# Kernel tuning notes

Measured on AMD Instinct MI355X. Metric: run time of the kernel, lower is better.

The kernel has to match this reference:

```python
import jax, jax.numpy as jnp
import numpy as np
from jax import lax

V, E, H, MLP, NCLS = 50000, 100, 100, 300, 3
B, T, C = 256, 128, 255


def _lstm_dir(x, Wih, Whh, bih, bhh, reverse):
    # x: [T, B, E]; PyTorch gate order i, f, g, o
    Bsz = x.shape[1]
    h0 = jnp.zeros((Bsz, H), x.dtype)
    c0 = jnp.zeros((Bsz, H), x.dtype)

    def step(carry, xt):
        h, c = carry
        gates = xt @ Wih.T + h @ Whh.T + (bih + bhh)  # [B, 4H]
        i, f, g, o = jnp.split(gates, 4, axis=-1)
        c = jax.nn.sigmoid(f) * c + jax.nn.sigmoid(i) * jnp.tanh(g)
        h = jax.nn.sigmoid(o) * jnp.tanh(c)
        return (h, c), h

    _, hs = lax.scan(step, (h0, c0), x, reverse=reverse)
    return hs  # [T, B, H]


def setup_inputs() -> dict:
    key = jax.random.key(0)
    ks = jax.random.split(key, 16)
    s_e = 1.0 / np.sqrt(H)
    inp = {
        "x": jax.random.randint(ks[0], (B, T), 0, V),
        "paths": jax.random.randint(ks[1], (B, C, 3), 0, T),
        "emb": jax.random.normal(ks[2], (V, E), jnp.float32),
        "Wih_f": jax.random.uniform(ks[3], (4 * H, E), jnp.float32, -s_e, s_e),
        "Whh_f": jax.random.uniform(ks[4], (4 * H, H), jnp.float32, -s_e, s_e),
        "bih_f": jax.random.uniform(ks[5], (4 * H,), jnp.float32, -s_e, s_e),
        "bhh_f": jax.random.uniform(ks[6], (4 * H,), jnp.float32, -s_e, s_e),
        "Wih_b": jax.random.uniform(ks[7], (4 * H, E), jnp.float32, -s_e, s_e),
        "Whh_b": jax.random.uniform(ks[8], (4 * H, H), jnp.float32, -s_e, s_e),
        "bih_b": jax.random.uniform(ks[9], (4 * H,), jnp.float32, -s_e, s_e),
        "bhh_b": jax.random.uniform(ks[10], (4 * H,), jnp.float32, -s_e, s_e),
        "W1": jax.random.normal(ks[11], (6 * H, MLP), jnp.float32) * 0.05,
        "b1": jnp.zeros((MLP,), jnp.float32),
        "W2": jax.random.normal(ks[12], (MLP, NCLS), jnp.float32) * 0.05,
        "b2": jnp.zeros((NCLS,), jnp.float32),
    }
    return inp


def reference(x, paths, emb, Wih_f, Whh_f, bih_f, bhh_f, Wih_b, Whh_b, bih_b, bhh_b, W1, b1, W2, b2):
    # embedding lookup (dropout is eval-mode identity)
    xe = emb[x]                      # [B, T, E]
    xe = jnp.transpose(xe, (1, 0, 2))  # [T, B, E] (seq-major like packed LSTM)
    hf = _lstm_dir(xe, Wih_f, Whh_f, bih_f, bhh_f, reverse=False)
    hb = _lstm_dir(xe, Wih_b, Whh_b, bih_b, bhh_b, reverse=True)
    h = jnp.concatenate([hf, hb], axis=-1)        # [T, B, 2H]
    hbt = jnp.transpose(h, (1, 0, 2))             # [B, T, 2H]
    # gather 3 positions per configuration; index -1 -> zero vector
    idx = jnp.clip(paths, 0, T - 1)               # [B, C, 3]
    g = hbt[jnp.arange(hbt.shape[0])[:, None, None], idx]  # [B, C, 3, 2H]
    g = jnp.where((paths >= 0)[..., None], g, 0.0)
    mlp_in = g.reshape(-1, 6 * H)                 # [B*C, 600]
    hdn = jnp.tanh(mlp_in @ W1 + b1)
    return jax.nn.softmax(hdn @ W2 + b2, axis=-1)  # [B*C, 3]
```

## Files before the change

### kernel.cpp

```cpp
#include <hip/hip_runtime.h>

typedef unsigned short u16;
typedef short short8 __attribute__((ext_vector_type(8)));
typedef float f32x4 __attribute__((ext_vector_type(4)));

__device__ __forceinline__ u16 f2b(float x){
  union{float f; unsigned u;} v; v.f = x;
  unsigned r = (v.u + 0x7FFFu + ((v.u >> 16) & 1u)) >> 16;
  return (u16)r;
}
__device__ __forceinline__ u16 f2h(float x){
  union{_Float16 h; u16 u;} c; c.h = (_Float16)x; return c.u;
}
__device__ __forceinline__ float b2f(u16 h){
  union{unsigned u; float f;} v; v.u = ((unsigned)h) << 16; return v.f;
}
__device__ __forceinline__ float sigm(float x){ return 1.0f/(1.0f + __expf(-x)); }
__device__ __forceinline__ float tanh_f(float x){ return 1.0f - 2.0f/(1.0f + __expf(2.0f*x)); }

__global__ void prep_kernel(const int* __restrict__ x, const float* __restrict__ emb,
   const float* __restrict__ Wih_f, const float* __restrict__ Whh_f,
   const float* __restrict__ bih_f, const float* __restrict__ bhh_f,
   const float* __restrict__ Wih_b, const float* __restrict__ Whh_b,
   const float* __restrict__ bih_b, const float* __restrict__ bhh_b,
   const float* __restrict__ W1,
   u16* __restrict__ xe, u16* __restrict__ wc, float* __restrict__ biasC,
   u16* __restrict__ whh2, u16* __restrict__ w1b, u16* __restrict__ hbt)
{
  int id = blockIdx.x*256 + threadIdx.x;
  const int N0 = 32768*128;
  const int N1 = 832*128;
  const int N2 = 800;
  const int N3 = 102400;
  const int N4 = 672*320;
  const int N5 = 32768*24;
  if (id < N0){
    int p = id >> 7, k = id & 127;
    float v = 0.f;
    if (k < 100) v = emb[x[p]*100 + k];
    xe[id] = f2b(v);
    return;
  }
  id -= N0;
  if (id < N1){
    int n = id >> 7, k = id & 127;
    float v = 0.f;
    if (k < 100){
      if (n < 400) v = Wih_f[n*100+k];
      else if (n < 800) v = Wih_b[(n-400)*100+k];
    }
    wc[id] = f2b(v);
    return;
  }
  id -= N1;
  if (id < N2){
    biasC[id] = (id < 400) ? (bih_f[id]+bhh_f[id]) : (bih_b[id-400]+bhh_b[id-400]);
    return;
  }
  id -= N2;
  if (id < N3){
    int d = id / 51200; int rem = id - d*51200;
    int t = rem >> 7;  int e  = rem & 127;
    int g = e >> 5;    int kq = e & 31;
    int u = t >> 2;    int q  = t & 3;
    int k = q*32 + kq;
    float v = 0.f;
    if (k < 100){
      const float* W = d ? Whh_b : Whh_f;
      v = W[(g*100 + u)*100 + k];
    }
    whh2[id] = f2h(v);
    return;
  }
  id -= N3;
  if (id < N4){
    int k = id / 320; int n = id - k*320;
    int seg = k / 224; int wwk = k - seg*224;
    float v = 0.f;
    if (n < 300 && wwk < 200) v = W1[(seg*200 + wwk)*300 + n];
    w1b[n*672 + k] = f2b(v);
    return;
  }
  id -= N4;
  if (id < N5){
    int p = id / 24; int k = id - p*24;
    hbt[p*224 + 200 + k] = 0;
  }
}

__global__ __launch_bounds__(256) void gemm1_kernel(const u16* __restrict__ xe,
    const u16* __restrict__ wc, const float* __restrict__ biasC, u16* __restrict__ inp)
{
  __shared__ __align__(16) u16 As[64*136];
  __shared__ __align__(16) u16 Bs[64*136];
  const int m0 = blockIdx.x*64, n0 = blockIdx.y*64;
  const int tid = threadIdx.x;
  #pragma unroll
  for (int i=0;i<4;i++){
    int f = i*256 + tid;
    int row = f >> 4, c8 = f & 15;
    *(uint4*)&As[row*136 + c8*8] = *(const uint4*)&xe[(m0+row)*128 + c8*8];
    *(uint4*)&Bs[row*136 + c8*8] = *(const uint4*)&wc[(n0+row)*128 + c8*8];
  }
  __syncthreads();
  const int w = tid >> 6, lane = tid & 63, col = lane & 15, quad = lane >> 4;
  f32x4 acc[4];
  #pragma unroll
  for (int nt=0;nt<4;nt++) acc[nt] = (f32x4){0.f,0.f,0.f,0.f};
  #pragma unroll
  for (int kc=0;kc<4;kc++){
    short8 af = *(const short8*)&As[(w*16+col)*136 + kc*32 + quad*8];
    #pragma unroll
    for (int nt=0;nt<4;nt++){
      short8 bfrag = *(const short8*)&Bs[(nt*16+col)*136 + kc*32 + quad*8];
      acc[nt] = __builtin_amdgcn_mfma_f32_16x16x32_bf16(af, bfrag, acc[nt], 0, 0, 0);
    }
  }
  #pragma unroll
  for (int nt=0;nt<4;nt++){
    int n = n0 + nt*16 + col;
    if (n < 800){
      float bs = biasC[n];
      int dir = (n >= 400) ? 1 : 0;
      int j = n - dir*400;
      int gg = j / 100, uu = j - gg*100;
      int pj = uu*4 + gg;
      #pragma unroll
      for (int r=0;r<4;r++){
        int m = m0 + w*16 + quad*4 + r;
        inp[(dir*32768 + m)*400 + pj] = f2b(acc[nt][r] + bs);
      }
    }
  }
}

#define DSL(CNT, H0,H1,H2,H3, A0,A1,A2,A3, B0,B1,B2,B3, C0,C1,C2,C3, D0,D1,D2,D3) \
  "s_waitcnt lgkmcnt(" #CNT ")\n\t" \
  "v_dot2_f32_f16 v16, v" #A0 ", v" #H0 ", v16\n\t" \
  "v_dot2_f32_f16 v17, v" #B0 ", v" #H0 ", v17\n\t" \
  "v_dot2_f32_f16 v18, v" #C0 ", v" #H0 ", v18\n\t" \
  "v_dot2_f32_f16 v19, v" #D0 ", v" #H0 ", v19\n\t" \
  "v_dot2_f32_f16 v16, v" #A1 ", v" #H1 ", v16\n\t" \
  "v_dot2_f32_f16 v17, v" #B1 ", v" #H1 ", v17\n\t" \
  "v_dot2_f32_f16 v18, v" #C1 ", v" #H1 ", v18\n\t" \
  "v_dot2_f32_f16 v19, v" #D1 ", v" #H1 ", v19\n\t" \
  "v_dot2_f32_f16 v16, v" #A2 ", v" #H2 ", v16\n\t" \
  "v_dot2_f32_f16 v17, v" #B2 ", v" #H2 ", v17\n\t" \
  "v_dot2_f32_f16 v18, v" #C2 ", v" #H2 ", v18\n\t" \
  "v_dot2_f32_f16 v19, v" #D2 ", v" #H2 ", v19\n\t" \
  "v_dot2_f32_f16 v16, v" #A3 ", v" #H3 ", v16\n\t" \
  "v_dot2_f32_f16 v17, v" #B3 ", v" #H3 ", v17\n\t" \
  "v_dot2_f32_f16 v18, v" #C3 ", v" #H3 ", v18\n\t" \
  "v_dot2_f32_f16 v19, v" #D3 ", v" #H3 ", v19\n\t"

__global__ __launch_bounds__(448) void lstm_kernel(const u16* __restrict__ inp,
    const u16* __restrict__ whh2, u16* __restrict__ hbt)
{
  __shared__ __align__(512) u16 hs2[256];
  const int cid = blockIdx.x;
  const int b = cid & 255, dir = cid >> 8;
  const int tid = threadIdx.x;
  for (int i = tid; i < 128; i += 448) ((float*)hs2)[i] = 0.f;
  __syncthreads();
  if (tid < 400){
    unsigned long long fe  = __ballot(1);
    unsigned long long g0e = __ballot((tid & 3) == 0);
    unsigned long long g1e = __ballot((tid & 3) == 1);
    const int sw  = tid >> 6;
    const int t0  = dir ? 127 : 0;
    const int dIb = dir ? -800 : 800;
    const int dHb = dir ? -448 : 448;
    const int swb = dir*102400;
    const unsigned sio = (unsigned)((dir*32768 + b*128 + t0)*400) * 2u;
    const unsigned sho = (unsigned)((b*128 + t0)*224 + dir*100) * 2u;
    const unsigned sra = (unsigned)(size_t)&hs2[0];
    const unsigned sha = sra + 256u;
    asm volatile(
      "v_mbcnt_lo_u32_b32 v0, -1, 0\n\t"
      "v_mbcnt_hi_u32_b32 v0, -1, v0\n\t"
      "v_lshl_add_u32 v0, %[sw], 6, v0\n\t"
      "v_lshlrev_b32 v1, 8, v0\n\t"
      "v_add_u32 v1, %[swb], v1\n\t"
      "v_lshrrev_b32 v3, 2, v0\n\t"
      "v_and_b32 v2, 3, v0\n\t"
      "v_lshl_add_u32 v23, v2, 6, %[sra]\n\t"
      "v_lshl_add_u32 v24, v3, 1, %[sha]\n\t"
      "v_lshl_add_u32 v25, v3, 1, %[sho]\n\t"
      "v_lshl_add_u32 v26, v3, 3, %[sio]\n\t"
      "v_mov_b32 v22, 0\n\t"
      "s_mov_b32 s20, 128\n\t"
      "global_load_dwordx2 v[20:21], v26, %[ib]\n\t"
      "v_add_u32 v26, %[dis], v26\n\t"
      "global_load_dwordx4 v[32:35], v1, %[wb]\n\t"
      "global_load_dwordx4 v[36:39], v1, %[wb] offset:16\n\t"
      "global_load_dwordx4 v[40:43], v1, %[wb] offset:32\n\t"
      "global_load_dwordx4 v[44:47], v1, %[wb] offset:48\n\t"
      "global_load_dwordx4 v[48:51], v1, %[wb] offset:64\n\t"
      "global_load_dwordx4 v[52:55], v1, %[wb] offset:80\n\t"
      "global_load_dwordx4 v[56:59], v1, %[wb] offset:96\n\t"
      "global_load_dwordx4 v[60:63], v1, %[wb] offset:112\n\t"
      "global_load_dwordx4 v[64:67], v1, %[wb] offset:128\n\t"
      "global_load_dwordx4 v[68:71], v1, %[wb] offset:144\n\t"
      "global_load_dwordx4 v[72:75], v1, %[wb] offset:160\n\t"
      "global_load_dwordx4 v[76:79], v1, %[wb] offset:176\n\t"
      "global_load_dwordx4 v[80:83], v1, %[wb] offset:192\n\t"
      "global_load_dwordx4 v[84:87], v1, %[wb] offset:208\n\t"
      "global_load_dwordx4 v[88:91], v1, %[wb] offset:224\n\t"
      "global_load_dwordx4 v[92:95], v1, %[wb] offset:240\n\t"
      "LSTM_T%=:\n\t"
      "s_waitcnt vmcnt(0)\n\t"
      "v_lshlrev_b32 v27, 16, v20\n\t"
      "v_and_b32 v28, 0xffff0000, v20\n\t"
      "v_lshlrev_b32 v29, 16, v21\n\t"
      "v_and_b32 v30, 0xffff0000, v21\n\t"
      "global_load_dwordx2 v[20:21], v26, %[ib]\n\t"
      "v_add_u32 v26, %[dis], v26\n\t"
      "ds_read_b128 v[0:3], v23\n\t"
      "ds_read_b128 v[4:7], v23 offset:16\n\t"
      "ds_read_b128 v[8:11], v23 offset:32\n\t"
      "ds_read_b128 v[12:15], v23 offset:48\n\t"
      "v_mov_b32 v16, 0\n\t"
      "v_mov_b32 v17, 0\n\t"
      "v_mov_b32 v18, 0\n\t"
      "v_mov_b32 v19, 0\n\t"
      DSL(3, 0,1,2,3,     32,33,34,35, 48,49,50,51, 64,65,66,67, 80,81,82,83)
      DSL(2, 4,5,6,7,     36,37,38,39, 52,53,54,55, 68,69,70,71, 84,85,86,87)
      DSL(1, 8,9,10,11,   40,41,42,43, 56,57,58,59, 72,73,74,75, 88,89,90,91)
      DSL(0, 12,13,14,15, 44,45,46,47, 60,61,62,63, 76,77,78,79, 92,93,94,95)
      "s_nop 1\n\t"
      "v_add_f32_dpp v16, v16, v16 quad_perm:[1,0,3,2] row_mask:0xf bank_mask:0xf\n\t"
      "v_add_f32_dpp v17, v17, v17 quad_perm:[1,0,3,2] row_mask:0xf bank_mask:0xf\n\t"
      "v_add_f32_dpp v18, v18, v18 quad_perm:[1,0,3,2] row_mask:0xf bank_mask:0xf\n\t"
      "v_add_f32_dpp v19, v19, v19 quad_perm:[1,0,3,2] row_mask:0xf bank_mask:0xf\n\t"
      "v_add_f32_dpp v16, v16, v16 quad_perm:[2,3,0,1] row_mask:0xf bank_mask:0xf\n\t"
      "v_add_f32_dpp v17, v17, v17 quad_perm:[2,3,0,1] row_mask:0xf bank_mask:0xf\n\t"
      "v_add_f32_dpp v18, v18, v18 quad_perm:[2,3,0,1] row_mask:0xf bank_mask:0xf\n\t"
      "v_add_f32_dpp v19, v19, v19 quad_perm:[2,3,0,1] row_mask:0xf bank_mask:0xf\n\t"
      "v_add_f32 v16, v16, v27\n\t"
      "v_add_f32 v17, v17, v28\n\t"
      "v_add_f32 v18, v18, v29\n\t"
      "v_add_f32 v19, v19, v30\n\t"
      "v_mul_f32 v27, 0xbfb8aa3b, v17\n\t"
      "v_mul_f32 v28, 0xbfb8aa3b, v16\n\t"
      "v_mul_f32 v29, 0x4038aa3b, v18\n\t"
      "v_exp_f32 v27, v27\n\t"
      "v_exp_f32 v28, v28\n\t"
      "v_exp_f32 v29, v29\n\t"
      "v_add_f32 v27, 1.0, v27\n\t"
      "v_add_f32 v28, 1.0, v28\n\t"
      "v_add_f32 v29, 1.0, v29\n\t"
      "v_rcp_f32 v27, v27\n\t"
      "v_rcp_f32 v28, v28\n\t"
      "v_rcp_f32 v29, v29\n\t"
      "v_mov_b32 v30, 1.0\n\t"
      "v_fmac_f32 v30, -2.0, v29\n\t"
      "v_mul_f32 v28, v28, v30\n\t"
      "v_fmac_f32 v28, v27, v22\n\t"
      "v_mov_b32 v22, v28\n\t"
      "v_mul_f32 v27, 0x4038aa3b, v22\n\t"
      "v_mul_f32 v29, 0xbfb8aa3b, v19\n\t"
      "v_exp_f32 v27, v27\n\t"
      "v_exp_f32 v29, v29\n\t"
      "v_add_f32 v27, 1.0, v27\n\t"
      "v_add_f32 v29, 1.0, v29\n\t"
      "v_rcp_f32 v27, v27\n\t"
      "v_rcp_f32 v29, v29\n\t"
      "v_mov_b32 v30, 1.0\n\t"
      "v_fmac_f32 v30, -2.0, v27\n\t"
      "v_mul_f32 v28, v29, v30\n\t"
      "v_cvt_pk_bf16_f32 v29, v28, v28\n\t"
      "v_cvt_f16_f32 v27, v28\n\t"
      "s_mov_b64 exec, %[g0e]\n\t"
      "ds_write_b16 v24, v27\n\t"
      "s_mov_b64 exec, %[g1e]\n\t"
      "global_store_short v25, v29, %[hb]\n\t"
      "s_mov_b64 exec, %[fe]\n\t"
      "v_add_u32 v25, %[dhs], v25\n\t"
      "v_xor_b32 v23, 0x100, v23\n\t"
      "v_xor_b32 v24, 0x100, v24\n\t"
      "s_waitcnt lgkmcnt(0)\n\t"
      "s_barrier\n\t"
      "s_sub_u32 s20, s20, 1\n\t"
      "s_cmp_lg_u32 s20, 0\n\t"
      "s_cbranch_scc1 LSTM_T%=\n\t"
      :
      : [sw]"s"(sw), [swb]"s"(swb),
        [sio]"s"(sio), [sho]"s"(sho), [sra]"s"(sra), [sha]"s"(sha),
        [wb]"s"(whh2), [ib]"s"(inp), [hb]"s"(hbt),
        [dis]"s"(dIb), [dhs]"s"(dHb),
        [fe]"s"(fe), [g0e]"s"(g0e), [g1e]"s"(g1e)
      : "memory","scc","s20",
        "v0","v1","v2","v3","v4","v5","v6","v7","v8","v9",
        "v10","v11","v12","v13","v14","v15","v16","v17","v18","v19",
        "v20","v21","v22","v23","v24","v25","v26","v27","v28","v29",
        "v30","v31","v32","v33","v34","v35","v36","v37","v38","v39",
        "v40","v41","v42","v43","v44","v45","v46","v47","v48","v49",
        "v50","v51","v52","v53","v54","v55","v56","v57","v58","v59",
        "v60","v61","v62","v63","v64","v65","v66","v67","v68","v69",
        "v70","v71","v72","v73","v74","v75","v76","v77","v78","v79",
        "v80","v81","v82","v83","v84","v85","v86","v87","v88","v89",
        "v90","v91","v92","v93","v94","v95"
    );
  }
}

__global__ __launch_bounds__(512) void mlp_kernel(const u16* __restrict__ hbt,
    const u16* __restrict__ w1b, const int* __restrict__ paths,
    const float* __restrict__ b1, const float* __restrict__ W2,
    const float* __restrict__ b2, float* __restrict__ out)
{
  __shared__ __align__(16) u16 As[128*40];
  __shared__ __align__(16) u16 Bs[320*40];
  const int m0 = blockIdx.x*128;
  const int tid = threadIdx.x;
  const int arow = tid >> 2, ac8 = tid & 3;
  const int am = m0 + arow;
  const int ab = am / 255;
  const int w = tid >> 6, lane = tid & 63, col = lane & 15, quad = lane >> 4;
  f32x4 acc[20];
  #pragma unroll
  for (int nt=0;nt<20;nt++) acc[nt] = (f32x4){0.f,0.f,0.f,0.f};
  for (int kc=0;kc<21;kc++){
    __syncthreads();
    for (int f = tid; f < 1280; f += 512){
      int br = f >> 2, bc = f & 3;
      *(uint4*)&Bs[br*40 + bc*8] = *(const uint4*)&w1b[br*672 + kc*32 + bc*8];
    }
    int seg = (kc >= 14) ? 2 : (kc >= 7 ? 1 : 0);
    int ko = kc - seg*7;
    int it = paths[am*3 + seg];
    uint4 v = make_uint4(0u,0u,0u,0u);
    if (it >= 0){
      int t = it > 127 ? 127 : it;
      v = *(const uint4*)&hbt[(ab*128 + t)*224 + ko*32 + ac8*8];
    }
    *(uint4*)&As[arow*40 + ac8*8] = v;
    __syncthreads();
    short8 af = *(const short8*)&As[(w*16+col)*40 + quad*8];
    #pragma unroll
    for (int nt=0;nt<20;nt++){
      short8 bfrag = *(const short8*)&Bs[(nt*16+col)*40 + quad*8];
      acc[nt] = __builtin_amdgcn_mfma_f32_16x16x32_bf16(af, bfrag, acc[nt], 0, 0, 0);
    }
  }
  float pz[4][3];
  #pragma unroll
  for (int r=0;r<4;r++){ pz[r][0]=0.f; pz[r][1]=0.f; pz[r][2]=0.f; }
  #pragma unroll
  for (int nt=0;nt<20;nt++){
    int n = nt*16 + col;
    if (n < 300){
      float bb = b1[n];
      float w20 = W2[n*3+0], w21 = W2[n*3+1], w22 = W2[n*3+2];
      #pragma unroll
      for (int r=0;r<4;r++){
        float hdn = tanh_f(acc[nt][r] + bb);
        pz[r][0] = fmaf(hdn, w20, pz[r][0]);
        pz[r][1] = fmaf(hdn, w21, pz[r][1]);
        pz[r][2] = fmaf(hdn, w22, pz[r][2]);
      }
    }
  }
  #pragma unroll
  for (int off=1; off<16; off<<=1){
    #pragma unroll
    for (int r=0;r<4;r++){
      pz[r][0] += __shfl_xor(pz[r][0], off, 64);
      pz[r][1] += __shfl_xor(pz[r][1], off, 64);
      pz[r][2] += __shfl_xor(pz[r][2], off, 64);
    }
  }
  float c0 = b2[0], c1 = b2[1], c2 = b2[2];
  #pragma unroll
  for (int r=0;r<4;r++){
    float z0 = pz[r][0]+c0, z1 = pz[r][1]+c1, z2 = pz[r][2]+c2;
    float mx = fmaxf(z0, fmaxf(z1, z2));
    float e0 = __expf(z0-mx), e1 = __expf(z1-mx), e2 = __expf(z2-mx);
    float inv = 1.0f/(e0+e1+e2);
    if (col < 3){
      float pv = (col==0 ? e0 : (col==1 ? e1 : e2)) * inv;
      out[(m0 + w*16 + quad*4 + r)*3 + col] = pv;
    }
  }
}

extern "C" void kernel_launch(void* const* d_in, const int* in_sizes, int n_in,
                              void* d_out, int out_size, void* d_ws, size_t ws_size,
                              hipStream_t stream)
{
  const int*   x     = (const int*)  d_in[0];
  const int*   paths = (const int*)  d_in[1];
  const float* emb   = (const float*)d_in[2];
  const float* Wih_f = (const float*)d_in[3];
  const float* Whh_f = (const float*)d_in[4];
  const float* bih_f = (const float*)d_in[5];
  const float* bhh_f = (const float*)d_in[6];
  const float* Wih_b = (const float*)d_in[7];
  const float* Whh_b = (const float*)d_in[8];
  const float* bih_b = (const float*)d_in[9];
  const float* bhh_b = (const float*)d_in[10];
  const float* W1    = (const float*)d_in[11];
  const float* b1    = (const float*)d_in[12];
  const float* W2    = (const float*)d_in[13];
  const float* b2    = (const float*)d_in[14];
  float* out = (float*)d_out;

  char* ws = (char*)d_ws;
  u16*   xe    = (u16*)  (ws + 0);
  u16*   wc    = (u16*)  (ws + 8388608);
  float* biasC = (float*)(ws + 8601600);
  u16*   whh2  = (u16*)  (ws + 8604800);
  u16*   w1b   = (u16*)  (ws + 8809600);
  u16*   inp   = (u16*)  (ws + 9239680);
  u16*   hbt   = (u16*)  (ws + 61668480);

  const int prep_total = 32768*128 + 832*128 + 800 + 102400 + 672*320 + 32768*24;
  prep_kernel<<<(prep_total + 255)/256, 256, 0, stream>>>(
      x, emb, Wih_f, Whh_f, bih_f, bhh_f, Wih_b, Whh_b, bih_b, bhh_b, W1,
      xe, wc, biasC, whh2, w1b, hbt);
  gemm1_kernel<<<dim3(512, 13), 256, 0, stream>>>(xe, wc, biasC, inp);
  lstm_kernel<<<512, 448, 0, stream>>>(inp, whh2, hbt);
  mlp_kernel<<<510, 512, 0, stream>>>(hbt, w1b, paths, b1, W2, b2, out);
}
```

Before: 373.4 us.

## Restructure LSTM recurrence to one thread per hidden unit with full-K dot products

The LSTM kernel now gives each lane a whole hidden unit (all four gates over all K), instead of splitting K across four lanes and reducing with DPP. Blocks shrink from 448 to 128 threads. Each thread keeps 208 VGPRs of fp16 recurrent weights resident and streams h from LDS in chunks. The aim is to remove the cross-lane reductions and the per-gate exec-mask juggling, and to cut per-step barrier cost with fewer waves. The cost is four times more serial dot2 work per lane per step and much higher register pressure, which limits occupancy.

```diff
diff --git a/kernel.cpp b/kernel.cpp
--- a/kernel.cpp
+++ b/kernel.cpp
@@ -25,13 +25,13 @@
    const float* __restrict__ bih_b, const float* __restrict__ bhh_b,
    const float* __restrict__ W1,
    u16* __restrict__ xe, u16* __restrict__ wc, float* __restrict__ biasC,
-   u16* __restrict__ whh2, u16* __restrict__ w1b, u16* __restrict__ hbt)
+   u16* __restrict__ whhU, u16* __restrict__ w1b, u16* __restrict__ hbt)
 {
   int id = blockIdx.x*256 + threadIdx.x;
   const int N0 = 32768*128;
   const int N1 = 832*128;
   const int N2 = 800;
-  const int N3 = 102400;
+  const int N3 = 106496;
   const int N4 = 672*320;
   const int N5 = 32768*24;
   if (id < N0){
@@ -59,17 +59,15 @@
   }
   id -= N2;
   if (id < N3){
-    int d = id / 51200; int rem = id - d*51200;
-    int t = rem >> 7;  int e  = rem & 127;
-    int g = e >> 5;    int kq = e & 31;
-    int u = t >> 2;    int q  = t & 3;
-    int k = q*32 + kq;
+    int d = id / 53248; int rem = id - d*53248;
+    int u = rem / 416;  int r2 = rem - u*416;
+    int g = r2 / 104;   int k = r2 - g*104;
     float v = 0.f;
-    if (k < 100){
+    if (u < 100 && k < 100){
       const float* W = d ? Whh_b : Whh_f;
       v = W[(g*100 + u)*100 + k];
     }
-    whh2[id] = f2h(v);
+    whhU[id] = f2h(v);
     return;
   }
   id -= N3;
@@ -134,174 +132,211 @@
   }
 }
 
-#define DSL(CNT, H0,H1,H2,H3, A0,A1,A2,A3, B0,B1,B2,B3, C0,C1,C2,C3, D0,D1,D2,D3) \
-  "s_waitcnt lgkmcnt(" #CNT ")\n\t" \
-  "v_dot2_f32_f16 v16, v" #A0 ", v" #H0 ", v16\n\t" \
-  "v_dot2_f32_f16 v17, v" #B0 ", v" #H0 ", v17\n\t" \
-  "v_dot2_f32_f16 v18, v" #C0 ", v" #H0 ", v18\n\t" \
-  "v_dot2_f32_f16 v19, v" #D0 ", v" #H0 ", v19\n\t" \
-  "v_dot2_f32_f16 v16, v" #A1 ", v" #H1 ", v16\n\t" \
-  "v_dot2_f32_f16 v17, v" #B1 ", v" #H1 ", v17\n\t" \
-  "v_dot2_f32_f16 v18, v" #C1 ", v" #H1 ", v18\n\t" \
-  "v_dot2_f32_f16 v19, v" #D1 ", v" #H1 ", v19\n\t" \
-  "v_dot2_f32_f16 v16, v" #A2 ", v" #H2 ", v16\n\t" \
-  "v_dot2_f32_f16 v17, v" #B2 ", v" #H2 ", v17\n\t" \
-  "v_dot2_f32_f16 v18, v" #C2 ", v" #H2 ", v18\n\t" \
-  "v_dot2_f32_f16 v19, v" #D2 ", v" #H2 ", v19\n\t" \
-  "v_dot2_f32_f16 v16, v" #A3 ", v" #H3 ", v16\n\t" \
-  "v_dot2_f32_f16 v17, v" #B3 ", v" #H3 ", v17\n\t" \
-  "v_dot2_f32_f16 v18, v" #C3 ", v" #H3 ", v18\n\t" \
-  "v_dot2_f32_f16 v19, v" #D3 ", v" #H3 ", v19\n\t"
-
-__global__ __launch_bounds__(448) void lstm_kernel(const u16* __restrict__ inp,
-    const u16* __restrict__ whh2, u16* __restrict__ hbt)
+#define DOT4(W0,W1,W2,W3,H) \
+  "v_dot2_f32_f16 v16, v" #W0 ", v" #H ", v16\n\t" \
+  "v_dot2_f32_f16 v17, v" #W1 ", v" #H ", v17\n\t" \
+  "v_dot2_f32_f16 v18, v" #W2 ", v" #H ", v18\n\t" \
+  "v_dot2_f32_f16 v19, v" #W3 ", v" #H ", v19\n\t"
+
+__global__ __launch_bounds__(128, 1) void lstm_kernel(const u16* __restrict__ inp,
+    const u16* __restrict__ whhU, u16* __restrict__ hbt)
 {
   __shared__ __align__(512) u16 hs2[256];
   const int cid = blockIdx.x;
   const int b = cid & 255, dir = cid >> 8;
   const int tid = threadIdx.x;
-  for (int i = tid; i < 128; i += 448) ((float*)hs2)[i] = 0.f;
+  ((float*)hs2)[tid] = 0.f;
   __syncthreads();
-  if (tid < 400){
-    unsigned long long fe  = __ballot(1);
-    unsigned long long g0e = __ballot((tid & 3) == 0);
-    unsigned long long g1e = __ballot((tid & 3) == 1);
-    const int sw  = tid >> 6;
-    const int t0  = dir ? 127 : 0;
-    const int dIb = dir ? -800 : 800;
-    const int dHb = dir ? -448 : 448;
-    const int swb = dir*102400;
-    const unsigned sio = (unsigned)((dir*32768 + b*128 + t0)*400) * 2u;
-    const unsigned sho = (unsigned)((b*128 + t0)*224 + dir*100) * 2u;
-    const unsigned sra = (unsigned)(size_t)&hs2[0];
-    const unsigned sha = sra + 256u;
-    asm volatile(
-      "v_mbcnt_lo_u32_b32 v0, -1, 0\n\t"
-      "v_mbcnt_hi_u32_b32 v0, -1, v0\n\t"
-      "v_lshl_add_u32 v0, %[sw], 6, v0\n\t"
-      "v_lshlrev_b32 v1, 8, v0\n\t"
-      "v_add_u32 v1, %[swb], v1\n\t"
-      "v_lshrrev_b32 v3, 2, v0\n\t"
-      "v_and_b32 v2, 3, v0\n\t"
-      "v_lshl_add_u32 v23, v2, 6, %[sra]\n\t"
-      "v_lshl_add_u32 v24, v3, 1, %[sha]\n\t"
-      "v_lshl_add_u32 v25, v3, 1, %[sho]\n\t"
-      "v_lshl_add_u32 v26, v3, 3, %[sio]\n\t"
-      "v_mov_b32 v22, 0\n\t"
-      "s_mov_b32 s20, 128\n\t"
-      "global_load_dwordx2 v[20:21], v26, %[ib]\n\t"
-      "v_add_u32 v26, %[dis], v26\n\t"
-      "global_load_dwordx4 v[32:35], v1, %[wb]\n\t"
-      "global_load_dwordx4 v[36:39], v1, %[wb] offset:16\n\t"
-      "global_load_dwordx4 v[40:43], v1, %[wb] offset:32\n\t"
-      "global_load_dwordx4 v[44:47], v1, %[wb] offset:48\n\t"
-      "global_load_dwordx4 v[48:51], v1, %[wb] offset:64\n\t"
-      "global_load_dwordx4 v[52:55], v1, %[wb] offset:80\n\t"
-      "global_load_dwordx4 v[56:59], v1, %[wb] offset:96\n\t"
-      "global_load_dwordx4 v[60:63], v1, %[wb] offset:112\n\t"
-      "global_load_dwordx4 v[64:67], v1, %[wb] offset:128\n\t"
-      "global_load_dwordx4 v[68:71], v1, %[wb] offset:144\n\t"
-      "global_load_dwordx4 v[72:75], v1, %[wb] offset:160\n\t"
-      "global_load_dwordx4 v[76:79], v1, %[wb] offset:176\n\t"
-      "global_load_dwordx4 v[80:83], v1, %[wb] offset:192\n\t"
-      "global_load_dwordx4 v[84:87], v1, %[wb] offset:208\n\t"
-      "global_load_dwordx4 v[88:91], v1, %[wb] offset:224\n\t"
-      "global_load_dwordx4 v[92:95], v1, %[wb] offset:240\n\t"
-      "LSTM_T%=:\n\t"
-      "s_waitcnt vmcnt(0)\n\t"
-      "v_lshlrev_b32 v27, 16, v20\n\t"
-      "v_and_b32 v28, 0xffff0000, v20\n\t"
-      "v_lshlrev_b32 v29, 16, v21\n\t"
-      "v_and_b32 v30, 0xffff0000, v21\n\t"
-      "global_load_dwordx2 v[20:21], v26, %[ib]\n\t"
-      "v_add_u32 v26, %[dis], v26\n\t"
-      "ds_read_b128 v[0:3], v23\n\t"
-      "ds_read_b128 v[4:7], v23 offset:16\n\t"
-      "ds_read_b128 v[8:11], v23 offset:32\n\t"
-      "ds_read_b128 v[12:15], v23 offset:48\n\t"
-      "v_mov_b32 v16, 0\n\t"
-      "v_mov_b32 v17, 0\n\t"
-      "v_mov_b32 v18, 0\n\t"
-      "v_mov_b32 v19, 0\n\t"
-      DSL(3, 0,1,2,3,     32,33,34,35, 48,49,50,51, 64,65,66,67, 80,81,82,83)
-      DSL(2, 4,5,6,7,     36,37,38,39, 52,53,54,55, 68,69,70,71, 84,85,86,87)
-      DSL(1, 8,9,10,11,   40,41,42,43, 56,57,58,59, 72,73,74,75, 88,89,90,91)
-      DSL(0, 12,13,14,15, 44,45,46,47, 60,61,62,63, 76,77,78,79, 92,93,94,95)
-      "s_nop 1\n\t"
-      "v_add_f32_dpp v16, v16, v16 quad_perm:[1,0,3,2] row_mask:0xf bank_mask:0xf\n\t"
-      "v_add_f32_dpp v17, v17, v17 quad_perm:[1,0,3,2] row_mask:0xf bank_mask:0xf\n\t"
-      "v_add_f32_dpp v18, v18, v18 quad_perm:[1,0,3,2] row_mask:0xf bank_mask:0xf\n\t"
-      "v_add_f32_dpp v19, v19, v19 quad_perm:[1,0,3,2] row_mask:0xf bank_mask:0xf\n\t"
-      "v_add_f32_dpp v16, v16, v16 quad_perm:[2,3,0,1] row_mask:0xf bank_mask:0xf\n\t"
-      "v_add_f32_dpp v17, v17, v17 quad_perm:[2,3,0,1] row_mask:0xf bank_mask:0xf\n\t"
-      "v_add_f32_dpp v18, v18, v18 quad_perm:[2,3,0,1] row_mask:0xf bank_mask:0xf\n\t"
-      "v_add_f32_dpp v19, v19, v19 quad_perm:[2,3,0,1] row_mask:0xf bank_mask:0xf\n\t"
-      "v_add_f32 v16, v16, v27\n\t"
-      "v_add_f32 v17, v17, v28\n\t"
-      "v_add_f32 v18, v18, v29\n\t"
-      "v_add_f32 v19, v19, v30\n\t"
-      "v_mul_f32 v27, 0xbfb8aa3b, v17\n\t"
-      "v_mul_f32 v28, 0xbfb8aa3b, v16\n\t"
-      "v_mul_f32 v29, 0x4038aa3b, v18\n\t"
-      "v_exp_f32 v27, v27\n\t"
-      "v_exp_f32 v28, v28\n\t"
-      "v_exp_f32 v29, v29\n\t"
-      "v_add_f32 v27, 1.0, v27\n\t"
-      "v_add_f32 v28, 1.0, v28\n\t"
-      "v_add_f32 v29, 1.0, v29\n\t"
-      "v_rcp_f32 v27, v27\n\t"
-      "v_rcp_f32 v28, v28\n\t"
-      "v_rcp_f32 v29, v29\n\t"
-      "v_mov_b32 v30, 1.0\n\t"
-      "v_fmac_f32 v30, -2.0, v29\n\t"
-      "v_mul_f32 v28, v28, v30\n\t"
-      "v_fmac_f32 v28, v27, v22\n\t"
-      "v_mov_b32 v22, v28\n\t"
-      "v_mul_f32 v27, 0x4038aa3b, v22\n\t"
-      "v_mul_f32 v29, 0xbfb8aa3b, v19\n\t"
-      "v_exp_f32 v27, v27\n\t"
-      "v_exp_f32 v29, v29\n\t"
-      "v_add_f32 v27, 1.0, v27\n\t"
-      "v_add_f32 v29, 1.0, v29\n\t"
-      "v_rcp_f32 v27, v27\n\t"
-      "v_rcp_f32 v29, v29\n\t"
-      "v_mov_b32 v30, 1.0\n\t"
-      "v_fmac_f32 v30, -2.0, v27\n\t"
-      "v_mul_f32 v28, v29, v30\n\t"
-      "v_cvt_pk_bf16_f32 v29, v28, v28\n\t"
-      "v_cvt_f16_f32 v27, v28\n\t"
-      "s_mov_b64 exec, %[g0e]\n\t"
-      "ds_write_b16 v24, v27\n\t"
-      "s_mov_b64 exec, %[g1e]\n\t"
-      "global_store_short v25, v29, %[hb]\n\t"
-      "s_mov_b64 exec, %[fe]\n\t"
-      "v_add_u32 v25, %[dhs], v25\n\t"
-      "v_xor_b32 v23, 0x100, v23\n\t"
-      "v_xor_b32 v24, 0x100, v24\n\t"
-      "s_waitcnt lgkmcnt(0)\n\t"
-      "s_barrier\n\t"
-      "s_sub_u32 s20, s20, 1\n\t"
-      "s_cmp_lg_u32 s20, 0\n\t"
-      "s_cbranch_scc1 LSTM_T%=\n\t"
-      :
-      : [sw]"s"(sw), [swb]"s"(swb),
-        [sio]"s"(sio), [sho]"s"(sho), [sra]"s"(sra), [sha]"s"(sha),
-        [wb]"s"(whh2), [ib]"s"(inp), [hb]"s"(hbt),
-        [dis]"s"(dIb), [dhs]"s"(dHb),
-        [fe]"s"(fe), [g0e]"s"(g0e), [g1e]"s"(g1e)
-      : "memory","scc","s20",
-        "v0","v1","v2","v3","v4","v5","v6","v7","v8","v9",
-        "v10","v11","v12","v13","v14","v15","v16","v17","v18","v19",
-        "v20","v21","v22","v23","v24","v25","v26","v27","v28","v29",
-        "v30","v31","v32","v33","v34","v35","v36","v37","v38","v39",
-        "v40","v41","v42","v43","v44","v45","v46","v47","v48","v49",
-        "v50","v51","v52","v53","v54","v55","v56","v57","v58","v59",
-        "v60","v61","v62","v63","v64","v65","v66","v67","v68","v69",
-        "v70","v71","v72","v73","v74","v75","v76","v77","v78","v79",
-        "v80","v81","v82","v83","v84","v85","v86","v87","v88","v89",
-        "v90","v91","v92","v93","v94","v95"
-    );
-  }
+  unsigned long long se = __ballot(tid < 100);
+  const int sw  = tid >> 6;
+  const int t0  = dir ? 127 : 0;
+  const int dIb = dir ? -800 : 800;
+  const int dHb = dir ? -448 : 448;
+  const int swb = dir*106496;
+  const unsigned sio = (unsigned)((dir*32768 + b*128 + t0)*400) * 2u;
+  const unsigned sho = (unsigned)((b*128 + t0)*224 + dir*100) * 2u;
+  const unsigned sra = (unsigned)(size_t)&hs2[0];
+  const unsigned sha = sra + 256u;
+  asm volatile(
+    "v_mbcnt_lo_u32_b32 v22, -1, 0\n\t"
+    "v_mbcnt_hi_u32_b32 v22, -1, v22\n\t"
+    "v_lshl_add_u32 v22, %[sw], 6, v22\n\t"
+    "v_mul_u32_u24 v27, 832, v22\n\t"
+    "v_add_u32 v27, %[swb], v27\n\t"
+    "v_lshl_add_u32 v26, v22, 3, %[sio]\n\t"
+    "v_lshl_add_u32 v25, v22, 1, %[sho]\n\t"
+    "v_lshl_add_u32 v24, v22, 1, %[sha]\n\t"
+    "v_mov_b32 v23, %[sra]\n\t"
+    "v_mov_b32 v30, 0\n\t"
+    "s_mov_b32 s20, 128\n\t"
+    "global_load_dwordx2 v[20:21], v26, %[ib]\n\t"
+    "v_add_u32 v26, %[dis], v26\n\t"
+    "global_load_dwordx4 v[32:35], v27, %[wb]\n\t"
+    "global_load_dwordx4 v[36:39], v27, %[wb] offset:16\n\t"
+    "global_load_dwordx4 v[40:43], v27, %[wb] offset:32\n\t"
+    "global_load_dwordx4 v[44:47], v27, %[wb] offset:48\n\t"
+    "global_load_dwordx4 v[48:51], v27, %[wb] offset:64\n\t"
+    "global_load_dwordx4 v[52:55], v27, %[wb] offset:80\n\t"
+    "global_load_dwordx4 v[56:59], v27, %[wb] offset:96\n\t"
+    "global_load_dwordx4 v[60:63], v27, %[wb] offset:112\n\t"
+    "global_load_dwordx4 v[64:67], v27, %[wb] offset:128\n\t"
+    "global_load_dwordx4 v[68:71], v27, %[wb] offset:144\n\t"
+    "global_load_dwordx4 v[72:75], v27, %[wb] offset:160\n\t"
+    "global_load_dwordx4 v[76:79], v27, %[wb] offset:176\n\t"
+    "global_load_dwordx4 v[80:83], v27, %[wb] offset:192\n\t"
+    "global_load_dwordx4 v[84:87],  v27, %[wb] offset:208\n\t"
+    "global_load_dwordx4 v[88:91],  v27, %[wb] offset:224\n\t"
+    "global_load_dwordx4 v[92:95],  v27, %[wb] offset:240\n\t"
+    "global_load_dwordx4 v[96:99],  v27, %[wb] offset:256\n\t"
+    "global_load_dwordx4 v[100:103], v27, %[wb] offset:272\n\t"
+    "global_load_dwordx4 v[104:107], v27, %[wb] offset:288\n\t"
+    "global_load_dwordx4 v[108:111], v27, %[wb] offset:304\n\t"
+    "global_load_dwordx4 v[112:115], v27, %[wb] offset:320\n\t"
+    "global_load_dwordx4 v[116:119], v27, %[wb] offset:336\n\t"
+    "global_load_dwordx4 v[120:123], v27, %[wb] offset:352\n\t"
+    "global_load_dwordx4 v[124:127], v27, %[wb] offset:368\n\t"
+    "global_load_dwordx4 v[128:131], v27, %[wb] offset:384\n\t"
+    "global_load_dwordx4 v[132:135], v27, %[wb] offset:400\n\t"
+    "global_load_dwordx4 v[136:139], v27, %[wb] offset:416\n\t"
+    "global_load_dwordx4 v[140:143], v27, %[wb] offset:432\n\t"
+    "global_load_dwordx4 v[144:147], v27, %[wb] offset:448\n\t"
+    "global_load_dwordx4 v[148:151], v27, %[wb] offset:464\n\t"
+    "global_load_dwordx4 v[152:155], v27, %[wb] offset:480\n\t"
+    "global_load_dwordx4 v[156:159], v27, %[wb] offset:496\n\t"
+    "global_load_dwordx4 v[160:163], v27, %[wb] offset:512\n\t"
+    "global_load_dwordx4 v[164:167], v27, %[wb] offset:528\n\t"
+    "global_load_dwordx4 v[168:171], v27, %[wb] offset:544\n\t"
+    "global_load_dwordx4 v[172:175], v27, %[wb] offset:560\n\t"
+    "global_load_dwordx4 v[176:179], v27, %[wb] offset:576\n\t"
+    "global_load_dwordx4 v[180:183], v27, %[wb] offset:592\n\t"
+    "global_load_dwordx4 v[184:187], v27, %[wb] offset:608\n\t"
+    "global_load_dwordx4 v[188:191], v27, %[wb] offset:624\n\t"
+    "global_load_dwordx4 v[192:195], v27, %[wb] offset:640\n\t"
+    "global_load_dwordx4 v[196:199], v27, %[wb] offset:656\n\t"
+    "global_load_dwordx4 v[200:203], v27, %[wb] offset:672\n\t"
+    "global_load_dwordx4 v[204:207], v27, %[wb] offset:688\n\t"
+    "global_load_dwordx4 v[208:211], v27, %[wb] offset:704\n\t"
+    "global_load_dwordx4 v[212:215], v27, %[wb] offset:720\n\t"
+    "global_load_dwordx4 v[216:219], v27, %[wb] offset:736\n\t"
+    "global_load_dwordx4 v[220:223], v27, %[wb] offset:752\n\t"
+    "global_load_dwordx4 v[224:227], v27, %[wb] offset:768\n\t"
+    "global_load_dwordx4 v[228:231], v27, %[wb] offset:784\n\t"
+    "global_load_dwordx4 v[232:235], v27, %[wb] offset:800\n\t"
+    "global_load_dwordx4 v[236:239], v27, %[wb] offset:816\n\t"
+    "LSTM_T%=:\n\t"
+    "s_waitcnt vmcnt(0)\n\t"
+    "v_lshlrev_b32 v16, 16, v20\n\t"
+    "v_and_b32 v17, 0xffff0000, v20\n\t"
+    "v_lshlrev_b32 v18, 16, v21\n\t"
+    "v_and_b32 v19, 0xffff0000, v21\n\t"
+    "global_load_dwordx2 v[20:21], v26, %[ib]\n\t"
+    "v_add_u32 v26, %[dis], v26\n\t"
+    "ds_read_b128 v[0:3], v23\n\t"
+    "ds_read_b128 v[4:7], v23 offset:16\n\t"
+    "ds_read_b128 v[8:11], v23 offset:32\n\t"
+    "ds_read_b128 v[12:15], v23 offset:48\n\t"
+    "s_waitcnt lgkmcnt(2)\n\t"
+    DOT4(32,84,136,188, 0) DOT4(33,85,137,189, 1) DOT4(34,86,138,190, 2) DOT4(35,87,139,191, 3)
+    DOT4(36,88,140,192, 4) DOT4(37,89,141,193, 5) DOT4(38,90,142,194, 6) DOT4(39,91,143,195, 7)
+    "ds_read_b128 v[0:3], v23 offset:64\n\t"
+    "ds_read_b128 v[4:7], v23 offset:80\n\t"
+    "s_waitcnt lgkmcnt(2)\n\t"
+    DOT4(40,92,144,196, 8)  DOT4(41,93,145,197, 9)  DOT4(42,94,146,198, 10) DOT4(43,95,147,199, 11)
+    DOT4(44,96,148,200, 12) DOT4(45,97,149,201, 13) DOT4(46,98,150,202, 14) DOT4(47,99,151,203, 15)
+    "ds_read_b128 v[8:11], v23 offset:96\n\t"
+    "ds_read_b128 v[12:15], v23 offset:112\n\t"
+    "s_waitcnt lgkmcnt(2)\n\t"
+    DOT4(48,100,152,204, 0) DOT4(49,101,153,205, 1) DOT4(50,102,154,206, 2) DOT4(51,103,155,207, 3)
+    DOT4(52,104,156,208, 4) DOT4(53,105,157,209, 5) DOT4(54,106,158,210, 6) DOT4(55,107,159,211, 7)
+    "ds_read_b128 v[0:3], v23 offset:128\n\t"
+    "ds_read_b128 v[4:7], v23 offset:144\n\t"
+    "s_waitcnt lgkmcnt(2)\n\t"
+    DOT4(56,108,160,212, 8)  DOT4(57,109,161,213, 9)  DOT4(58,110,162,214, 10) DOT4(59,111,163,215, 11)
+    DOT4(60,112,164,216, 12) DOT4(61,113,165,217, 13) DOT4(62,114,166,218, 14) DOT4(63,115,167,219, 15)
+    "ds_read_b128 v[8:11], v23 offset:160\n\t"
+    "ds_read_b128 v[12:15], v23 offset:176\n\t"
+    "s_waitcnt lgkmcnt(2)\n\t"
+    DOT4(64,116,168,220, 0) DOT4(65,117,169,221, 1) DOT4(66,118,170,222, 2) DOT4(67,119,171,223, 3)
+    DOT4(68,120,172,224, 4) DOT4(69,121,173,225, 5) DOT4(70,122,174,226, 6) DOT4(71,123,175,227, 7)
+    "ds_read_b128 v[0:3], v23 offset:192\n\t"
+    "s_waitcnt lgkmcnt(1)\n\t"
+    DOT4(72,124,176,228, 8)  DOT4(73,125,177,229, 9)  DOT4(74,126,178,230, 10) DOT4(75,127,179,231, 11)
+    DOT4(76,128,180,232, 12) DOT4(77,129,181,233, 13) DOT4(78,130,182,234, 14) DOT4(79,131,183,235, 15)
+    "s_waitcnt lgkmcnt(0)\n\t"
+    DOT4(80,132,184,236, 0) DOT4(81,133,185,237, 1) DOT4(82,134,186,238, 2) DOT4(83,135,187,239, 3)
+    "v_mul_f32 v27, 0xbfb8aa3b, v17\n\t"
+    "v_mul_f32 v28, 0xbfb8aa3b, v16\n\t"
+    "v_mul_f32 v29, 0x4038aa3b, v18\n\t"
+    "v_exp_f32 v27, v27\n\t"
+    "v_exp_f32 v28, v28\n\t"
+    "v_exp_f32 v29, v29\n\t"
+    "v_add_f32 v27, 1.0, v27\n\t"
+    "v_add_f32 v28, 1.0, v28\n\t"
+    "v_add_f32 v29, 1.0, v29\n\t"
+    "v_rcp_f32 v27, v27\n\t"
+    "v_rcp_f32 v28, v28\n\t"
+    "v_rcp_f32 v29, v29\n\t"
+    "v_mov_b32 v31, 1.0\n\t"
+    "v_fmac_f32 v31, -2.0, v29\n\t"
+    "v_mul_f32 v28, v28, v31\n\t"
+    "v_fmac_f32 v28, v27, v30\n\t"
+    "v_mov_b32 v30, v28\n\t"
+    "v_mul_f32 v27, 0x4038aa3b, v30\n\t"
+    "v_mul_f32 v29, 0xbfb8aa3b, v19\n\t"
+    "v_exp_f32 v27, v27\n\t"
+    "v_exp_f32 v29, v29\n\t"
+    "v_add_f32 v27, 1.0, v27\n\t"
+    "v_add_f32 v29, 1.0, v29\n\t"
+    "v_rcp_f32 v27, v27\n\t"
+    "v_rcp_f32 v29, v29\n\t"
+    "v_mov_b32 v31, 1.0\n\t"
+    "v_fmac_f32 v31, -2.0, v27\n\t"
+    "v_mul_f32 v28, v29, v31\n\t"
+    "v_cvt_pk_bf16_f32 v29, v28, v28\n\t"
+    "v_cvt_f16_f32 v27, v28\n\t"
+    "s_mov_b64 exec, %[se]\n\t"
+    "ds_write_b16 v24, v27\n\t"
+    "global_store_short v25, v29, %[hb]\n\t"
+    "s_mov_b64 exec, -1\n\t"
+    "v_add_u32 v25, %[dhs], v25\n\t"
+    "v_xor_b32 v23, 0x100, v23\n\t"
+    "v_xor_b32 v24, 0x100, v24\n\t"
+    "s_waitcnt lgkmcnt(0)\n\t"
+    "s_barrier\n\t"
+    "s_sub_u32 s20, s20, 1\n\t"
+    "s_cmp_lg_u32 s20, 0\n\t"
+    "s_cbranch_scc1 LSTM_T%=\n\t"
+    :
+    : [sw]"s"(sw), [swb]"s"(swb),
+      [sio]"s"(sio), [sho]"s"(sho), [sra]"s"(sra), [sha]"s"(sha),
+      [wb]"s"(whhU), [ib]"s"(inp), [hb]"s"(hbt),
+      [dis]"s"(dIb), [dhs]"s"(dHb), [se]"s"(se)
+    : "memory","scc","s20",
+      "v0","v1","v2","v3","v4","v5","v6","v7","v8","v9",
+      "v10","v11","v12","v13","v14","v15","v16","v17","v18","v19",
+      "v20","v21","v22","v23","v24","v25","v26","v27","v28","v29",
+      "v30","v31","v32","v33","v34","v35","v36","v37","v38","v39",
+      "v40","v41","v42","v43","v44","v45","v46","v47","v48","v49",
+      "v50","v51","v52","v53","v54","v55","v56","v57","v58","v59",
+      "v60","v61","v62","v63","v64","v65","v66","v67","v68","v69",
+      "v70","v71","v72","v73","v74","v75","v76","v77","v78","v79",
+      "v80","v81","v82","v83","v84","v85","v86","v87","v88","v89",
+      "v90","v91","v92","v93","v94","v95","v96","v97","v98","v99",
+      "v100","v101","v102","v103","v104","v105","v106","v107","v108","v109",
+      "v110","v111","v112","v113","v114","v115","v116","v117","v118","v119",
+      "v120","v121","v122","v123","v124","v125","v126","v127","v128","v129",
+      "v130","v131","v132","v133","v134","v135","v136","v137","v138","v139",
+      "v140","v141","v142","v143","v144","v145","v146","v147","v148","v149",
+      "v150","v151","v152","v153","v154","v155","v156","v157","v158","v159",
+      "v160","v161","v162","v163","v164","v165","v166","v167","v168","v169",
+      "v170","v171","v172","v173","v174","v175","v176","v177","v178","v179",
+      "v180","v181","v182","v183","v184","v185","v186","v187","v188","v189",
+      "v190","v191","v192","v193","v194","v195","v196","v197","v198","v199",
+      "v200","v201","v202","v203","v204","v205","v206","v207","v208","v209",
+      "v210","v211","v212","v213","v214","v215","v216","v217","v218","v219",
+      "v220","v221","v222","v223","v224","v225","v226","v227","v228","v229",
+      "v230","v231","v232","v233","v234","v235","v236","v237","v238","v239"
+  );
 }
 
 __global__ __launch_bounds__(512) void mlp_kernel(const u16* __restrict__ hbt,
@@ -409,16 +444,16 @@
   u16*   xe    = (u16*)  (ws + 0);
   u16*   wc    = (u16*)  (ws + 8388608);
   float* biasC = (float*)(ws + 8601600);
-  u16*   whh2  = (u16*)  (ws + 8604800);
-  u16*   w1b   = (u16*)  (ws + 8809600);
-  u16*   inp   = (u16*)  (ws + 9239680);
-  u16*   hbt   = (u16*)  (ws + 61668480);
-
-  const int prep_total = 32768*128 + 832*128 + 800 + 102400 + 672*320 + 32768*24;
+  u16*   whhU  = (u16*)  (ws + 8604800);
+  u16*   w1b   = (u16*)  (ws + 8817792);
+  u16*   inp   = (u16*)  (ws + 9247872);
+  u16*   hbt   = (u16*)  (ws + 61676672);
+
+  const int prep_total = 32768*128 + 832*128 + 800 + 106496 + 672*320 + 32768*24;
   prep_kernel<<<(prep_total + 255)/256, 256, 0, stream>>>(
       x, emb, Wih_f, Whh_f, bih_f, bhh_f, Wih_b, Whh_b, bih_b, bhh_b, W1,
-      xe, wc, biasC, whh2, w1b, hbt);
+      xe, wc, biasC, whhU, w1b, hbt);
   gemm1_kernel<<<dim3(512, 13), 256, 0, stream>>>(xe, wc, biasC, inp);
-  lstm_kernel<<<512, 448, 0, stream>>>(inp, whh2, hbt);
+  lstm_kernel<<<512, 128, 0, stream>>>(inp, whhU, hbt);
   mlp_kernel<<<510, 512, 0, stream>>>(hbt, w1b, paths, b1, W2, b2, out);
 }
```

Result: slower. 385.0 us (+3.1%).
